# Kernel optimization log

Hardware: AMD Instinct MI355X
Metric: run time of the kernel (lower is better)

The kernel has to match this reference:

```python
import jax, jax.numpy as jnp
import numpy as np

B, LQ, LK, DIM = 2, 2048, 2048, 1024
HEADS, DH = 8, 64
INNER = HEADS * DH  # 512


def setup_inputs() -> dict:
    key = jax.random.key(0)
    ks = jax.random.split(key, 7)
    x = jax.random.normal(ks[0], (B, LQ, DIM), dtype=jnp.float32)
    y = jax.random.normal(ks[1], (B, LK, DIM), dtype=jnp.float32)
    # binary mask, 1 => masked (gets -1e9 added)
    mask = jax.random.randint(ks[2], (B, LQ, LK), 0, 2).astype(jnp.float32)
    s = 0.02
    Wq = jax.random.normal(ks[3], (INNER, DIM), dtype=jnp.float32) * s
    Wk = jax.random.normal(ks[4], (INNER, DIM), dtype=jnp.float32) * s
    Wv = jax.random.normal(ks[5], (INNER, DIM), dtype=jnp.float32) * s
    Wo = jax.random.normal(ks[6], (DIM, INNER), dtype=jnp.float32) * s
    return {"x": x, "y": y, "mask": mask, "Wq": Wq, "Wk": Wk, "Wv": Wv, "Wo": Wo}


def reference(x, y, mask, Wq, Wk, Wv, Wo):
    scale = DH ** -0.5
    # projections (Linear without bias: x @ W.T)
    q = (x @ Wq.T) * scale            # [B, LQ, INNER]
    k = y @ Wk.T                      # [B, LK, INNER]
    v = y @ Wv.T                      # [B, LK, INNER]
    # split into heads (torch.split along last dim == reshape to [.., H, DH])
    q = q.reshape(B, LQ, HEADS, DH)
    k = k.reshape(B, LK, HEADS, DH)
    v = v.reshape(B, LK, HEADS, DH)
    # per-head QK^T + additive mask*-1e9, softmax over keys, then V
    scores = jnp.einsum('bqhd,bkhd->bhqk', q, k) + mask[:, None, :, :] * (-1e9)
    attn = jax.nn.softmax(scores, axis=-1)
    out = jnp.einsum('bhqk,bkhd->bqhd', attn, v).reshape(B, LQ, INNER)
    return out @ Wo.T                 # [B, LQ, DIM]
```

## Files before the change

### kernel.cpp

```cpp
#include <hip/hip_runtime.h>
#include <hip/hip_bf16.h>
#include <stdint.h>

#define BATCH 2
#define LQ 2048
#define LK 2048
#define DIM 1024
#define HEADS 8
#define DH 64
#define INNER 512

typedef __attribute__((ext_vector_type(8))) short short8;
typedef __attribute__((ext_vector_type(4))) float f32x4;

__device__ __forceinline__ float bf2f(unsigned short u) {
    union { unsigned int i; float f; } v;
    v.i = ((unsigned int)u) << 16;
    return v.f;
}
__device__ __forceinline__ unsigned short f2bf(float f) {
    __hip_bfloat16 h = __float2bfloat16(f);
    return *reinterpret_cast<unsigned short*>(&h);
}
__device__ __forceinline__ float fexp2(float x) {
#if __has_builtin(__builtin_amdgcn_exp2f)
    return __builtin_amdgcn_exp2f(x);
#else
    return __expf(x * 0.69314718056f);
#endif
}
__device__ __forceinline__ void stc(unsigned short* C, size_t i, float v) { C[i] = f2bf(v); }
__device__ __forceinline__ void stc(float* C, size_t i, float v) { C[i] = v; }

typedef __attribute__((address_space(1))) const unsigned int gu32;
typedef __attribute__((address_space(3))) unsigned int lu32;
__device__ __forceinline__ void gload16(const void* g, void* l) {
    __builtin_amdgcn_global_load_lds((gu32*)g, (lu32*)l, 16, 0, 0);
}

__global__ __launch_bounds__(256) void prep(
    const float* __restrict__ x,  const float* __restrict__ y,
    const float* __restrict__ wq, const float* __restrict__ wk,
    const float* __restrict__ wv, const float* __restrict__ wo,
    const float* __restrict__ mask,
    unsigned short* __restrict__ xb,  unsigned short* __restrict__ yb,
    unsigned short* __restrict__ wqb, unsigned short* __restrict__ wkb,
    unsigned short* __restrict__ wvb, unsigned short* __restrict__ wob,
    unsigned long long* __restrict__ mbits)
{
    if (blockIdx.y == 6) {
        const int wid = blockIdx.x * 4 + (threadIdx.x >> 6);
        const int lane = threadIdx.x & 63;
        for (int task = wid; task < BATCH * LQ * 8; task += 4096) {
            int row = task >> 3, g = task & 7;
            const float* mp = mask + (size_t)row * LK + g * 256;
            unsigned long long* ob = mbits + (size_t)row * (LK / 64) + g * 4;
            float v0 = mp[0 * 64 + lane];
            float v1 = mp[1 * 64 + lane];
            float v2 = mp[2 * 64 + lane];
            float v3 = mp[3 * 64 + lane];
            unsigned long long b0 = __ballot(v0 > 0.5f);
            unsigned long long b1 = __ballot(v1 > 0.5f);
            unsigned long long b2 = __ballot(v2 > 0.5f);
            unsigned long long b3 = __ballot(v3 > 0.5f);
            if (lane == 0) { ob[0] = b0; ob[1] = b1; ob[2] = b2; ob[3] = b3; }
        }
        return;
    }
    const float* src; unsigned short* dst; int n4;
    switch (blockIdx.y) {
        case 0: src = x;  dst = xb;  n4 = (BATCH * LQ * DIM) / 4; break;
        case 1: src = y;  dst = yb;  n4 = (BATCH * LK * DIM) / 4; break;
        case 2: src = wq; dst = wqb; n4 = (INNER * DIM) / 4; break;
        case 3: src = wk; dst = wkb; n4 = (INNER * DIM) / 4; break;
        case 4: src = wv; dst = wvb; n4 = (INNER * DIM) / 4; break;
        default: src = wo; dst = wob; n4 = (INNER * DIM) / 4; break;
    }
    const int stride = gridDim.x * 256;
    for (int i = blockIdx.x * 256 + threadIdx.x; i < n4; i += stride) {
        float4 f = ((const float4*)src)[i];
        ushort4 u;
        u.x = f2bf(f.x); u.y = f2bf(f.y); u.z = f2bf(f.z); u.w = f2bf(f.w);
        ((ushort4*)dst)[i] = u;
    }
}

template <int IM, int JN, typename TC, int EPI>
__device__ __forceinline__ void gemm_body(
    const unsigned short* __restrict__ A,
    const unsigned short* __restrict__ W,
    TC* __restrict__ C,
    int K, int N, float scale,
    unsigned short* As, unsigned short* Bs)
{
    constexpr int BM = IM * 32;
    constexpr int BN = JN * 32;
    constexpr int ACH = BM * 8;
    constexpr int BCH = BN * 8;
    constexpr int AUS = BM * 64;
    constexpr int BUS = BN * 64;

    const int tid = threadIdx.x;
    const int m0 = blockIdx.x * BM;
    const int n0 = blockIdx.y * BN;
    const int w = tid >> 6, lane = tid & 63;
    const int q4 = lane >> 4, l16 = lane & 15;
    const int wm = (w >> 1) * (IM * 16), wn = (w & 1) * (JN * 16);
    const int sw = l16 & 7;

    f32x4 acc[IM][JN] = {};

#pragma unroll
    for (int i = 0; i < ACH / 256; ++i) {
        int s = tid + i * 256;
        int r = s >> 3, ch = (s & 7) ^ (r & 7);
        gload16(A + (size_t)(m0 + r) * K + ch * 8, As + (size_t)s * 8);
    }
#pragma unroll
    for (int i = 0; i < BCH / 256; ++i) {
        int s = tid + i * 256;
        int r = s >> 3, ch = (s & 7) ^ (r & 7);
        gload16(W + (size_t)(n0 + r) * K + ch * 8, Bs + (size_t)s * 8);
    }
    __syncthreads();

    const int nt = K / 64;
    for (int t = 0; t < nt; ++t) {
        const int curA = (t & 1) * AUS;
        const int curB = (t & 1) * BUS;
        if (t + 1 < nt) {
            int kk = (t + 1) * 64;
            const int nxtA = AUS - curA, nxtB = BUS - curB;
#pragma unroll
            for (int i = 0; i < ACH / 256; ++i) {
                int s = tid + i * 256;
                int r = s >> 3, ch = (s & 7) ^ (r & 7);
                gload16(A + (size_t)(m0 + r) * K + kk + ch * 8, As + nxtA + (size_t)s * 8);
            }
#pragma unroll
            for (int i = 0; i < BCH / 256; ++i) {
                int s = tid + i * 256;
                int r = s >> 3, ch = (s & 7) ^ (r & 7);
                gload16(W + (size_t)(n0 + r) * K + kk + ch * 8, Bs + nxtB + (size_t)s * 8);
            }
        }

#pragma unroll
        for (int ks = 0; ks < 2; ++ks) {
            const int kq = ((ks * 4 + q4) ^ sw) * 8;
            short8 a[IM], b[JN];
#pragma unroll
            for (int i = 0; i < IM; ++i)
                a[i] = *(const short8*)(As + curA + (wm + i * 16 + l16) * 64 + kq);
#pragma unroll
            for (int j = 0; j < JN; ++j)
                b[j] = *(const short8*)(Bs + curB + (wn + j * 16 + l16) * 64 + kq);
#pragma unroll
            for (int i = 0; i < IM; ++i)
#pragma unroll
                for (int j = 0; j < JN; ++j)
                    acc[i][j] = __builtin_amdgcn_mfma_f32_16x16x32_bf16(
                        a[i], b[j], acc[i][j], 0, 0, 0);
        }
        __syncthreads();
    }

    if (EPI == 0) {
#pragma unroll
        for (int i = 0; i < IM; ++i)
#pragma unroll
            for (int j = 0; j < JN; ++j)
#pragma unroll
                for (int r = 0; r < 4; ++r) {
                    int row = m0 + wm + i * 16 + q4 * 4 + r;
                    int col = n0 + wn + j * 16 + l16;
                    stc(C, (size_t)row * N + col, acc[i][j][r] * scale);
                }
    } else {
        constexpr int KW = IM * 16;
        constexpr int DW = JN * 16;
        constexpr int TPS = KW + 8;
        unsigned short* TP = As + w * (DW * TPS);
#pragma unroll
        for (int i = 0; i < IM; ++i)
#pragma unroll
            for (int j = 0; j < JN; ++j) {
                ushort4 u;
                u.x = f2bf(acc[i][j][0]); u.y = f2bf(acc[i][j][1]);
                u.z = f2bf(acc[i][j][2]); u.w = f2bf(acc[i][j][3]);
                *(ushort4*)(TP + (j * 16 + l16) * TPS + i * 16 + q4 * 4) = u;
            }
        const int keyflat = m0 + wm;
        const int bb = keyflat >> 11, key0 = keyflat & (LK - 1);
        const int hh = (n0 + wn) >> 6;
        const int dlow = (n0 + wn) & 63;
        constexpr int RCH = KW / 8;
        constexpr int NCH = DW * RCH;
#pragma unroll
        for (int p = 0; p < NCH / 64; ++p) {
            int c = p * 64 + lane;
            int dl = c / RCH, kc = c % RCH;
            uint4 v = *(const uint4*)(TP + dl * TPS + kc * 8);
            *(uint4*)((unsigned short*)C +
                ((size_t)((bb * HEADS + hh) * DH + dlow + dl)) * LK + key0 + kc * 8) = v;
        }
    }
}

#define QSCALE 0.18033688011112042f

__global__ __launch_bounds__(256) void proj_qkv(
    const unsigned short* __restrict__ xb, const unsigned short* __restrict__ yb,
    const unsigned short* __restrict__ wqb, const unsigned short* __restrict__ wkb,
    const unsigned short* __restrict__ wvb,
    unsigned short* __restrict__ qb, unsigned short* __restrict__ kb,
    unsigned short* __restrict__ vt)
{
    __shared__ __align__(16) unsigned short As[2 * 128 * 64];
    __shared__ __align__(16) unsigned short Bs[2 * 64 * 64];
    const int z = blockIdx.z;
    const unsigned short* A = (z == 0) ? xb : yb;
    const unsigned short* W = (z == 0) ? wqb : (z == 1) ? wkb : wvb;
    if (z == 2)
        gemm_body<4, 2, unsigned short, 1>(A, W, vt, DIM, INNER, 1.0f, As, Bs);
    else
        gemm_body<4, 2, unsigned short, 0>(A, W, (z == 0) ? qb : kb, DIM, INNER,
                                           (z == 0) ? QSCALE : 1.0f, As, Bs);
}

__global__ __launch_bounds__(256) void gemm_out(
    const unsigned short* __restrict__ A,
    const unsigned short* __restrict__ W,
    float* __restrict__ C)
{
    __shared__ __align__(16) unsigned short As[2 * 128 * 64];
    __shared__ __align__(16) unsigned short Bs[2 * 64 * 64];
    gemm_body<4, 2, float, 0>(A, W, C, INNER, DIM, 1.0f, As, Bs);
}

#define AT_SLOT (64 * 64)

__global__ __launch_bounds__(512, 4) void attn_mfma(
    const unsigned short* __restrict__ Q,
    const unsigned short* __restrict__ Kb,
    const unsigned short* __restrict__ Vt,
    const unsigned long long* __restrict__ Mb,
    unsigned short* __restrict__ O)
{
    __shared__ __align__(16) unsigned short Ks[4 * AT_SLOT];
    __shared__ __align__(16) unsigned short Vs[4 * AT_SLOT];
    __shared__ __align__(16) unsigned short Ps[8 * 16 * 64];

    const int tid = threadIdx.x;
    const int q0 = blockIdx.x * 64;
    const int h = blockIdx.y, b = blockIdx.z;
    const int w = tid >> 6, lane = tid & 63;
    const int g = w & 3;
    const int par = w >> 2;
    const int q4 = lane >> 4, l16 = lane & 15;
    const int sw = l16 & 7;

    short8 qf[2];
    {
        const unsigned short* qp =
            Q + (size_t)(b * LQ + q0 + g * 16 + l16) * INNER + h * DH + q4 * 8;
        qf[0] = *(const short8*)(qp);
        qf[1] = *(const short8*)(qp + 32);
    }

    f32x4 o[4] = {};
    float lacc[4] = {0.f, 0.f, 0.f, 0.f};

    const unsigned short* kbase = Kb + (size_t)(b * LK) * INNER + h * DH;
    const unsigned short* vbase = Vt + (size_t)((b * HEADS + h) * DH) * LK;
    const unsigned long long* mrow =
        Mb + (size_t)(b * LQ + q0 + g * 16 + q4 * 4) * (LK / 64);

    const int rr = tid >> 3;
    const int ch = (tid & 7) ^ (rr & 7);

#pragma unroll
    for (int tn = 0; tn < 2; ++tn) {
        gload16(kbase + (size_t)(tn * 64 + rr) * INNER + ch * 8,
                Ks + tn * AT_SLOT + (size_t)tid * 8);
        gload16(vbase + (size_t)rr * LK + tn * 64 + ch * 8,
                Vs + tn * AT_SLOT + (size_t)tid * 8);
    }
    __syncthreads();

    const int NR = LK / 128;
    for (int rd = 0; rd < NR; ++rd) {
        if (rd + 1 < NR) {
#pragma unroll
            for (int i = 0; i < 2; ++i) {
                const int tn = 2 * rd + 2 + i;
                const int sl = tn & 3;
                gload16(kbase + (size_t)(tn * 64 + rr) * INNER + ch * 8,
                        Ks + sl * AT_SLOT + (size_t)tid * 8);
                gload16(vbase + (size_t)rr * LK + tn * 64 + ch * 8,
                        Vs + sl * AT_SLOT + (size_t)tid * 8);
            }
        }
        const int t = 2 * rd + par;
        const int cur = (t & 3) * AT_SLOT;

        f32x4 s[4];
#pragma unroll
        for (int j = 0; j < 4; ++j) {
            s[j] = f32x4{0.f, 0.f, 0.f, 0.f};
#pragma unroll
            for (int ks = 0; ks < 2; ++ks) {
                short8 kf = *(const short8*)(Ks + cur + (j * 16 + l16) * 64
                                             + (((ks * 4 + q4) ^ sw) * 8));
                s[j] = __builtin_amdgcn_mfma_f32_16x16x32_bf16(qf[ks], kf, s[j], 0, 0, 0);
            }
        }

#pragma unroll
        for (int r2 = 0; r2 < 4; ++r2) {
            unsigned long long bits = mrow[(size_t)r2 * (LK / 64) + t];
#pragma unroll
            for (int j = 0; j < 4; ++j) {
                float e = fexp2(s[j][r2]);
                float pe = ((bits >> (j * 16 + l16)) & 1ull) ? 0.f : e;
                s[j][r2] = pe;
                lacc[r2] += pe;
            }
        }

        unsigned short* Pw = Ps + w * 1024;
#pragma unroll
        for (int j = 0; j < 4; ++j)
#pragma unroll
            for (int r2 = 0; r2 < 4; ++r2) {
                const int row = q4 * 4 + r2;
                Pw[row * 64 + (((j * 2 + (l16 >> 3)) ^ (row & 7)) << 3) + (l16 & 7)]
                    = f2bf(s[j][r2]);
            }

#pragma unroll
        for (int ks = 0; ks < 2; ++ks) {
            short8 pf = *(const short8*)(Pw + l16 * 64 + (((ks * 4 + q4) ^ sw) << 3));
#pragma unroll
            for (int dd = 0; dd < 4; ++dd) {
                short8 vf = *(const short8*)(Vs + cur + (dd * 16 + l16) * 64
                                             + (((ks * 4 + q4) ^ sw) * 8));
                o[dd] = __builtin_amdgcn_mfma_f32_16x16x32_bf16(pf, vf, o[dd], 0, 0, 0);
            }
        }
        __syncthreads();
    }

    float* xch = (float*)Ks;
    if (par) {
        float* d = xch + (size_t)(g * 64 + lane) * 21;
#pragma unroll
        for (int dd = 0; dd < 4; ++dd)
#pragma unroll
            for (int r2 = 0; r2 < 4; ++r2) d[dd * 4 + r2] = o[dd][r2];
#pragma unroll
        for (int r2 = 0; r2 < 4; ++r2) d[16 + r2] = lacc[r2];
    }
    __syncthreads();
    if (!par) {
        const float* d = xch + (size_t)(g * 64 + lane) * 21;
#pragma unroll
        for (int dd = 0; dd < 4; ++dd)
#pragma unroll
            for (int r2 = 0; r2 < 4; ++r2) o[dd][r2] += d[dd * 4 + r2];
#pragma unroll
        for (int r2 = 0; r2 < 4; ++r2) lacc[r2] += d[16 + r2];

#pragma unroll
        for (int off = 1; off < 16; off <<= 1)
#pragma unroll
            for (int r2 = 0; r2 < 4; ++r2)
                lacc[r2] += __shfl_xor(lacc[r2], off);
        float inv[4];
#pragma unroll
        for (int r2 = 0; r2 < 4; ++r2) inv[r2] = 1.0f / lacc[r2];

#pragma unroll
        for (int dd = 0; dd < 4; ++dd)
#pragma unroll
            for (int r2 = 0; r2 < 4; ++r2) {
                int qrow = b * LQ + q0 + g * 16 + q4 * 4 + r2;
                int col = h * DH + dd * 16 + l16;
                O[(size_t)qrow * INNER + col] = f2bf(o[dd][r2] * inv[r2]);
            }
    }
}

extern "C" void kernel_launch(void* const* d_in, const int* in_sizes, int n_in,
                              void* d_out, int out_size, void* d_ws, size_t ws_size,
                              hipStream_t stream) {
    const float* x    = (const float*)d_in[0];
    const float* y    = (const float*)d_in[1];
    const float* mask = (const float*)d_in[2];
    const float* Wq   = (const float*)d_in[3];
    const float* Wk   = (const float*)d_in[4];
    const float* Wv   = (const float*)d_in[5];
    const float* Wo   = (const float*)d_in[6];
    float* out = (float*)d_out;

    const size_t NX = (size_t)BATCH * LQ * DIM;
    const size_t NS = (size_t)BATCH * LQ * INNER;
    const size_t NW = (size_t)INNER * DIM;
    unsigned short* xb  = (unsigned short*)d_ws;
    unsigned short* yb  = xb + NX;
    unsigned short* qb  = yb + NX;
    unsigned short* kb  = qb + NS;
    unsigned short* vt  = kb + NS;
    unsigned short* wqb = vt + NS;
    unsigned short* wkb = wqb + NW;
    unsigned short* wvb = wkb + NW;
    unsigned short* wob = wvb + NW;
    unsigned long long* mbits = (unsigned long long*)(wob + NW);
    unsigned short* ao  = xb;

    dim3 blk(256);
    prep<<<dim3(1024, 7), blk, 0, stream>>>(
        x, y, Wq, Wk, Wv, Wo, mask, xb, yb, wqb, wkb, wvb, wob, mbits);
    proj_qkv<<<dim3(4096 / 128, INNER / 64, 3), blk, 0, stream>>>(
        xb, yb, wqb, wkb, wvb, qb, kb, vt);
    attn_mfma<<<dim3(LQ / 64, HEADS, BATCH), dim3(512), 0, stream>>>(
        qb, kb, vt, mbits, ao);
    gemm_out<<<dim3(4096 / 128, DIM / 64), blk, 0, stream>>>(ao, wob, out);
}
```

Measured before the change: 183.7 us.

## Keep attention probabilities in registers via transposed MFMA and permlane swaps

The attention kernel now computes S^T by swapping the MFMA operands, so each lane holds four consecutive keys of a single query row. It packs the exp values to bf16 with v_cvt_pk_bf16_f32 and rearranges them into the PV operand layout with permlane32/16 swaps. This removes the per-wave LDS round trip for P and its shared buffer. Mask loads drop to one 64-bit word per lane, row sums reduce with two shuffles, and output stores become 4-wide vectors. The risk is correctness, which depends on the permlane lane mapping exactly matching the MFMA B-operand layout.

```diff
diff --git a/kernel.cpp b/kernel.cpp
--- a/kernel.cpp
+++ b/kernel.cpp
@@ -31,6 +31,28 @@
 }
 __device__ __forceinline__ void stc(unsigned short* C, size_t i, float v) { C[i] = f2bf(v); }
 __device__ __forceinline__ void stc(float* C, size_t i, float v) { C[i] = v; }
+
+__device__ __forceinline__ unsigned cvtpk_bf16(float lo, float hi) {
+    unsigned r;
+    asm("v_cvt_pk_bf16_f32 %0, %1, %2" : "=v"(r) : "v"(lo), "v"(hi));
+    return r;
+}
+__device__ __forceinline__ void perm32swap(unsigned& a, unsigned& b) {
+#if __has_builtin(__builtin_amdgcn_permlane32_swap)
+    auto r = __builtin_amdgcn_permlane32_swap(a, b, false, false);
+    a = r[0]; b = r[1];
+#else
+    asm volatile("v_permlane32_swap_b32 %0, %1" : "+v"(a), "+v"(b));
+#endif
+}
+__device__ __forceinline__ void perm16swap(unsigned& a, unsigned& b) {
+#if __has_builtin(__builtin_amdgcn_permlane16_swap)
+    auto r = __builtin_amdgcn_permlane16_swap(a, b, false, false);
+    a = r[0]; b = r[1];
+#else
+    asm volatile("v_permlane16_swap_b32 %0, %1" : "+v"(a), "+v"(b));
+#endif
+}
 
 typedef __attribute__((address_space(1))) const unsigned int gu32;
 typedef __attribute__((address_space(3))) unsigned int lu32;
@@ -167,7 +189,7 @@
 
     if (EPI == 0) {
 #pragma unroll
-        for (int i = 0; i < IM; ++i)
+    for (int i = 0; i < IM; ++i)
 #pragma unroll
             for (int j = 0; j < JN; ++j)
 #pragma unroll
@@ -249,7 +271,6 @@
 {
     __shared__ __align__(16) unsigned short Ks[4 * AT_SLOT];
     __shared__ __align__(16) unsigned short Vs[4 * AT_SLOT];
-    __shared__ __align__(16) unsigned short Ps[8 * 16 * 64];
 
     const int tid = threadIdx.x;
     const int q0 = blockIdx.x * 64;
@@ -269,12 +290,12 @@
     }
 
     f32x4 o[4] = {};
-    float lacc[4] = {0.f, 0.f, 0.f, 0.f};
+    float lacc = 0.f;
 
     const unsigned short* kbase = Kb + (size_t)(b * LK) * INNER + h * DH;
     const unsigned short* vbase = Vt + (size_t)((b * HEADS + h) * DH) * LK;
     const unsigned long long* mrow =
-        Mb + (size_t)(b * LQ + q0 + g * 16 + q4 * 4) * (LK / 64);
+        Mb + (size_t)(b * LQ + q0 + g * 16 + l16) * (LK / 64);
 
     const int rr = tid >> 3;
     const int ch = (tid & 7) ^ (rr & 7);
@@ -312,40 +333,43 @@
             for (int ks = 0; ks < 2; ++ks) {
                 short8 kf = *(const short8*)(Ks + cur + (j * 16 + l16) * 64
                                              + (((ks * 4 + q4) ^ sw) * 8));
-                s[j] = __builtin_amdgcn_mfma_f32_16x16x32_bf16(qf[ks], kf, s[j], 0, 0, 0);
-            }
-        }
-
-#pragma unroll
-        for (int r2 = 0; r2 < 4; ++r2) {
-            unsigned long long bits = mrow[(size_t)r2 * (LK / 64) + t];
-#pragma unroll
-            for (int j = 0; j < 4; ++j) {
-                float e = fexp2(s[j][r2]);
-                float pe = ((bits >> (j * 16 + l16)) & 1ull) ? 0.f : e;
-                s[j][r2] = pe;
-                lacc[r2] += pe;
-            }
-        }
-
-        unsigned short* Pw = Ps + w * 1024;
-#pragma unroll
-        for (int j = 0; j < 4; ++j)
-#pragma unroll
-            for (int r2 = 0; r2 < 4; ++r2) {
-                const int row = q4 * 4 + r2;
-                Pw[row * 64 + (((j * 2 + (l16 >> 3)) ^ (row & 7)) << 3) + (l16 & 7)]
-                    = f2bf(s[j][r2]);
-            }
-
+                s[j] = __builtin_amdgcn_mfma_f32_16x16x32_bf16(kf, qf[ks], s[j], 0, 0, 0);
+            }
+        }
+
+        unsigned long long bsh = mrow[t] >> (q4 * 4);
+        unsigned pk[8];
+#pragma unroll
+        for (int j = 0; j < 4; ++j) {
+            unsigned nib = (unsigned)(bsh >> (16 * j)) & 0xFu;
+            float p0 = (nib & 1u) ? 0.f : fexp2(s[j][0]);
+            float p1 = (nib & 2u) ? 0.f : fexp2(s[j][1]);
+            float p2 = (nib & 4u) ? 0.f : fexp2(s[j][2]);
+            float p3 = (nib & 8u) ? 0.f : fexp2(s[j][3]);
+            lacc += (p0 + p1) + (p2 + p3);
+            pk[2 * j]     = cvtpk_bf16(p0, p1);
+            pk[2 * j + 1] = cvtpk_bf16(p2, p3);
+        }
+
+        short8 pf[2];
 #pragma unroll
         for (int ks = 0; ks < 2; ++ks) {
-            short8 pf = *(const short8*)(Pw + l16 * 64 + (((ks * 4 + q4) ^ sw) << 3));
+            unsigned a0 = pk[4 * ks + 0], b0 = pk[4 * ks + 2];
+            unsigned a1 = pk[4 * ks + 1], b1 = pk[4 * ks + 3];
+            perm32swap(a0, b0); perm16swap(a0, b0);
+            perm32swap(a1, b1); perm16swap(a1, b1);
+            union { unsigned u[4]; short8 s8; } up;
+            up.u[0] = a0; up.u[1] = a1; up.u[2] = b0; up.u[3] = b1;
+            pf[ks] = up.s8;
+        }
+
+#pragma unroll
+        for (int ks = 0; ks < 2; ++ks) {
 #pragma unroll
             for (int dd = 0; dd < 4; ++dd) {
                 short8 vf = *(const short8*)(Vs + cur + (dd * 16 + l16) * 64
                                              + (((ks * 4 + q4) ^ sw) * 8));
-                o[dd] = __builtin_amdgcn_mfma_f32_16x16x32_bf16(pf, vf, o[dd], 0, 0, 0);
+                o[dd] = __builtin_amdgcn_mfma_f32_16x16x32_bf16(vf, pf[ks], o[dd], 0, 0, 0);
             }
         }
         __syncthreads();
@@ -353,41 +377,35 @@
 
     float* xch = (float*)Ks;
     if (par) {
-        float* d = xch + (size_t)(g * 64 + lane) * 21;
+        float* d = xch + (size_t)(g * 64 + lane) * 17;
 #pragma unroll
         for (int dd = 0; dd < 4; ++dd)
 #pragma unroll
             for (int r2 = 0; r2 < 4; ++r2) d[dd * 4 + r2] = o[dd][r2];
-#pragma unroll
-        for (int r2 = 0; r2 < 4; ++r2) d[16 + r2] = lacc[r2];
+        d[16] = lacc;
     }
     __syncthreads();
     if (!par) {
-        const float* d = xch + (size_t)(g * 64 + lane) * 21;
+        const float* d = xch + (size_t)(g * 64 + lane) * 17;
 #pragma unroll
         for (int dd = 0; dd < 4; ++dd)
 #pragma unroll
             for (int r2 = 0; r2 < 4; ++r2) o[dd][r2] += d[dd * 4 + r2];
-#pragma unroll
-        for (int r2 = 0; r2 < 4; ++r2) lacc[r2] += d[16 + r2];
-
-#pragma unroll
-        for (int off = 1; off < 16; off <<= 1)
-#pragma unroll
-            for (int r2 = 0; r2 < 4; ++r2)
-                lacc[r2] += __shfl_xor(lacc[r2], off);
-        float inv[4];
-#pragma unroll
-        for (int r2 = 0; r2 < 4; ++r2) inv[r2] = 1.0f / lacc[r2];
-
-#pragma unroll
-        for (int dd = 0; dd < 4; ++dd)
-#pragma unroll
-            for (int r2 = 0; r2 < 4; ++r2) {
-                int qrow = b * LQ + q0 + g * 16 + q4 * 4 + r2;
-                int col = h * DH + dd * 16 + l16;
-                O[(size_t)qrow * INNER + col] = f2bf(o[dd][r2] * inv[r2]);
-            }
+        lacc += d[16];
+
+        lacc += __shfl_xor(lacc, 16);
+        lacc += __shfl_xor(lacc, 32);
+        const float inv = 1.0f / lacc;
+
+        unsigned short* orow =
+            O + (size_t)(b * LQ + q0 + g * 16 + l16) * INNER + h * DH + q4 * 4;
+#pragma unroll
+        for (int dd = 0; dd < 4; ++dd) {
+            ushort4 u;
+            u.x = f2bf(o[dd][0] * inv); u.y = f2bf(o[dd][1] * inv);
+            u.z = f2bf(o[dd][2] * inv); u.w = f2bf(o[dd][3] * inv);
+            *(ushort4*)(orow + dd * 16) = u;
+        }
     }
 }
 
```

Result: faster. 179.4 us (-2.3%).
